# Performance work log

Measured on AMD Instinct MI355X. Metric: run time of the kernel, lower is better.

## Reference

```python
import jax, jax.numpy as jnp
import numpy as np

B, S, D = 2, 2048, 2048
H, KVH = 32, 8
HD = D // H          # 64
N_REP = H // KVH     # 4
NEG = -1e9


def setup_inputs() -> dict:
    key = jax.random.key(0)
    ks = jax.random.split(key, 5)
    x = jax.random.normal(ks[0], (B, S, D), dtype=jnp.float32)
    std = 0.02
    wq = jax.random.normal(ks[1], (H * HD, D), dtype=jnp.float32) * std
    wk = jax.random.normal(ks[2], (KVH * HD, D), dtype=jnp.float32) * std
    wv = jax.random.normal(ks[3], (KVH * HD, D), dtype=jnp.float32) * std
    wo = jax.random.normal(ks[4], (D, H * HD), dtype=jnp.float32) * std
    # RoPE tables: (S, HD//2)
    inv_freq = 1.0 / (10000.0 ** (np.arange(0, HD, 2, dtype=np.float32) / HD))
    t = np.arange(S, dtype=np.float32)
    freqs = np.outer(t, inv_freq)
    freqs_cos = jnp.asarray(np.cos(freqs))
    freqs_sin = jnp.asarray(np.sin(freqs))
    # additive causal mask [1,1,S,S]
    causal = np.tril(np.ones((S, S), dtype=bool))
    mask = jnp.asarray(np.where(causal, 0.0, NEG).astype(np.float32))[None, None]
    return {"x": x, "wq": wq, "wk": wk, "wv": wv, "wo": wo,
            "freqs_cos": freqs_cos, "freqs_sin": freqs_sin, "mask": mask}


def _apply_rope(t, cos, sin):
    # t: [B,S,nh,HD]; cos/sin: [S, HD//2]
    tr = t.reshape(t.shape[:-1] + (HD // 2, 2))
    r, i = tr[..., 0], tr[..., 1]
    c = cos[None, :, None, :]
    s = sin[None, :, None, :]
    out_r = r * c - i * s
    out_i = r * s + i * c
    return jnp.stack([out_r, out_i], axis=-1).reshape(t.shape)


def reference(x, wq, wk, wv, wo, freqs_cos, freqs_sin, mask):
    b, s, _ = x.shape
    q = (x @ wq.T).reshape(b, s, H, HD)
    k = (x @ wk.T).reshape(b, s, KVH, HD)
    v = (x @ wv.T).reshape(b, s, KVH, HD)
    q = _apply_rope(q, freqs_cos, freqs_sin)
    k = _apply_rope(k, freqs_cos, freqs_sin)
    # repeat_kv (GQA expansion) then move heads forward: [B,H,S,HD]
    k = jnp.repeat(k, N_REP, axis=2)
    v = jnp.repeat(v, N_REP, axis=2)
    q = q.transpose(0, 2, 1, 3)
    k = k.transpose(0, 2, 1, 3)
    v = v.transpose(0, 2, 1, 3)
    scale = 1.0 / jnp.sqrt(jnp.float32(HD))
    scores = jnp.einsum("bhqd,bhkd->bhqk", q, k) * scale + mask[:, :, :s, :s]
    attn = jax.nn.softmax(scores, axis=-1)
    out = jnp.einsum("bhqk,bhkd->bhqd", attn, v)
    out = out.transpose(0, 2, 1, 3).reshape(b, s, H * HD)
    return out @ wo.T
```

## Files before the change

### kernel.cpp

```cpp
#include <hip/hip_runtime.h>
#include <hip/hip_bf16.h>
#include <stdint.h>


#define NEG_BIG (-1e9f)
#define SCALE_LOG2 0.18033688011112042f
#define DEFER_THR 10.0f

typedef __bf16 bf16x8 __attribute__((ext_vector_type(8)));
typedef float f32x4 __attribute__((ext_vector_type(4)));
typedef float f32x16 __attribute__((ext_vector_type(16)));
typedef uint16_t u16x8 __attribute__((ext_vector_type(8)));
typedef uint32_t u32x4 __attribute__((ext_vector_type(4)));

__device__ inline uint16_t f2bf(float x) {
    __hip_bfloat16 h = __float2bfloat16(x);
    return __builtin_bit_cast(uint16_t, h);
}
__device__ inline float bf2f(uint16_t u) {
    uint32_t t = (uint32_t)u << 16;
    return __builtin_bit_cast(float, t);
}

__device__ inline void async_cp16(const void* g, void* l) {
    __builtin_amdgcn_global_load_lds(
        (const __attribute__((address_space(1))) uint32_t*)g,
        (__attribute__((address_space(3))) uint32_t*)l,
        16 , 0 , 0 );
}

__global__ void cvt4(const float* __restrict__ in, uint16_t* __restrict__ out, int n4) {
    int i = blockIdx.x * blockDim.x + threadIdx.x;
    if (i >= n4) return;
    const float4 v = ((const float4*)in)[i];
    ushort4 o;
    o.x = f2bf(v.x); o.y = f2bf(v.y); o.z = f2bf(v.z); o.w = f2bf(v.w);
    ((ushort4*)out)[i] = o;
}

__global__ void build_wqkv(const float* __restrict__ wq, const float* __restrict__ wk,
                           const float* __restrict__ wv, uint16_t* __restrict__ out) {
    int i = blockIdx.x * blockDim.x + threadIdx.x;
    if (i >= (3072 * 2048) / 4) return;
    int e = i * 4;
    int row = e >> 11;
    int col = e & 2047;
    const float* src = (row < 2048) ? (wq + (long)row * 2048 + col)
                     : (row < 2560) ? (wk + (long)(row - 2048) * 2048 + col)
                                    : (wv + (long)(row - 2560) * 2048 + col);
    const float4 v = *(const float4*)src;
    ushort4 o;
    o.x = f2bf(v.x); o.y = f2bf(v.y); o.z = f2bf(v.z); o.w = f2bf(v.w);
    ((ushort4*)(out + e))[0] = o;
}

template <int BN, int OUT_BF16>
__global__ __launch_bounds__(512) void gemm256(const uint16_t* __restrict__ A,
                                               const uint16_t* __restrict__ Bw,
                                               void* __restrict__ Cout,
                                               int M, int N, int K) {
    constexpr int WN = BN / 4;
    constexpr int NF = WN / 16;
    constexpr int BROUNDS = BN / 64;

    __shared__ __align__(16) uint16_t As[2][256 * 64];
    __shared__ __align__(16) uint16_t Bs[2][BN * 64];

    const int tid = threadIdx.x;
    const int l = tid & 63;
    const int w = tid >> 6;
    const int wmi = w >> 2;
    const int wni = w & 3;
    const int c = l & 15, g = l >> 4;
    const long row0 = (long)blockIdx.x * 256;
    const long col0 = (long)blockIdx.y * BN;

    f32x4 acc[8][NF] = {};

    auto STAGE = [&](int buf, int t) {
        const long k0 = (long)t * 64;
#pragma unroll
        for (int rr = 0; rr < 4; ++rr) {
            const int e = rr * 512 + tid;
            const int r = e >> 3;
            const int gs = (e & 7) ^ (r & 7);
            async_cp16(A + (row0 + r) * (long)K + k0 + gs * 8, &As[buf][e * 8]);
        }
#pragma unroll
        for (int rr = 0; rr < BROUNDS; ++rr) {
            const int e = rr * 512 + tid;
            const int r = e >> 3;
            const int gs = (e & 7) ^ (r & 7);
            async_cp16(Bw + (col0 + r) * (long)K + k0 + gs * 8, &Bs[buf][e * 8]);
        }
    };

    STAGE(0, 0);
    __syncthreads();

    const int nt = K / 64;
    for (int t = 0; t < nt; ++t) {
        const int cur = t & 1;
        if (t + 1 < nt) STAGE(cur ^ 1, t + 1);

#pragma unroll
        for (int kk = 0; kk < 2; ++kk) {
            bf16x8 bF[NF];
#pragma unroll
            for (int n = 0; n < NF; ++n) {
                const int rb = wni * WN + n * 16 + c;
                const int sp = ((kk * 4 + g) ^ (c & 7));
                bF[n] = *(const bf16x8*)&Bs[cur][rb * 64 + sp * 8];
            }
#pragma unroll
            for (int mh = 0; mh < 2; ++mh) {
                bf16x8 aF[4];
#pragma unroll
                for (int mm = 0; mm < 4; ++mm) {
                    const int ra = wmi * 128 + (mh * 4 + mm) * 16 + c;
                    const int sp = ((kk * 4 + g) ^ (c & 7));
                    aF[mm] = *(const bf16x8*)&As[cur][ra * 64 + sp * 8];
                }
                __builtin_amdgcn_s_setprio(1);
#pragma unroll
                for (int mm = 0; mm < 4; ++mm)
#pragma unroll
                    for (int n = 0; n < NF; ++n)
                        acc[mh * 4 + mm][n] = __builtin_amdgcn_mfma_f32_16x16x32_bf16(
                            aF[mm], bF[n], acc[mh * 4 + mm][n], 0, 0, 0);
                __builtin_amdgcn_s_setprio(0);
            }
        }
        if (t + 1 < nt) __syncthreads();
    }

#pragma unroll
    for (int m = 0; m < 8; ++m) {
        const long rg = row0 + wmi * 128 + m * 16 + g * 4;
#pragma unroll
        for (int n = 0; n < NF; ++n) {
            const long cg = col0 + wni * WN + n * 16 + c;
#pragma unroll
            for (int r = 0; r < 4; ++r) {
                float v = acc[m][n][r];
                if (OUT_BF16)
                    ((uint16_t*)Cout)[(rg + r) * (long)N + cg] = f2bf(v);
                else
                    ((float*)Cout)[(rg + r) * (long)N + cg] = v;
            }
        }
    }
}

__global__ void rope_q(uint16_t* __restrict__ qkv,
                       const float* __restrict__ cosT,
                       const float* __restrict__ sinT) {
    int idx = blockIdx.x * blockDim.x + threadIdx.x;
    if (idx >= 4096 * 1024) return;
    int m = idx >> 10;
    int j = idx & 1023;
    int s = m & 2047;
    int d2 = j & 31;
    float cc = cosT[s * 32 + d2];
    float ss = sinT[s * 32 + d2];
    uint32_t* p = (uint32_t*)(qkv + (long)m * 3072 + 2 * j);
    uint32_t v = *p;
    float re = bf2f((uint16_t)(v & 0xffffu));
    float im = bf2f((uint16_t)(v >> 16));
    float orr = re * cc - im * ss;
    float oi = re * ss + im * cc;
    *p = (uint32_t)f2bf(orr) | ((uint32_t)f2bf(oi) << 16);
}

__global__ void kpack_rope(const uint16_t* __restrict__ qkv,
                           const float* __restrict__ cosT,
                           const float* __restrict__ sinT,
                           uint16_t* __restrict__ Kpk) {
    const int wid = (blockIdx.x * blockDim.x + threadIdx.x) >> 6;
    const int l = threadIdx.x & 63;
    const int lq = l & 31, hi = l >> 5;
    const int s = wid & 3;
    const int tile = (wid >> 2) & 63;
    const int bk = wid >> 8;
    const int b = bk >> 3, kvh = bk & 7;
    const int key = 32 * tile + lq;
    const uint16_t* src = qkv + (long)(b * 2048 + key) * 3072
                        + 2048 + kvh * 64 + 16 * s + 8 * hi;
    u16x8 v = *(const u16x8*)src;
    const int d2b = 8 * s + 4 * hi;
    u16x8 o;
#pragma unroll
    for (int p = 0; p < 4; ++p) {
        const float cc = cosT[key * 32 + d2b + p];
        const float ss = sinT[key * 32 + d2b + p];
        const float re = bf2f(v[2 * p]);
        const float im = bf2f(v[2 * p + 1]);
        o[2 * p]     = f2bf(re * cc - im * ss);
        o[2 * p + 1] = f2bf(re * ss + im * cc);
    }
    *(u16x8*)(Kpk + (((long)(bk * 64 + tile) * 4 + s) * 64 + l) * 8) = o;
}

__global__ void vpack_direct(const uint16_t* __restrict__ qkv, uint16_t* __restrict__ Vpk) {
    const int wid = (blockIdx.x * blockDim.x + threadIdx.x) >> 6;
    const int l = threadIdx.x & 63;
    const int lq = l & 31, hi = l >> 5;
    const int s2 = wid & 1;
    const int nd = (wid >> 1) & 1;
    const int tile = (wid >> 2) & 63;
    const int bk = wid >> 8;
    const int b = bk >> 3, kvh = bk & 7;
    const int key0 = 32 * tile + 16 * s2 + 8 * hi;
    const uint16_t* src = qkv + (long)(b * 2048 + key0) * 3072
                        + 2560 + kvh * 64 + nd * 32 + lq;
    u16x8 v;
#pragma unroll
    for (int jj = 0; jj < 8; ++jj) v[jj] = src[(long)jj * 3072];
    *(u16x8*)(Vpk + ((((long)(bk * 64 + tile) * 2 + nd) * 2 + s2) * 64 + l) * 8) = v;
}

__device__ inline void pack_pf(const float pr[16], int hi, bf16x8 pf[2]) {
    uint32_t wds[8], xw[8];
#pragma unroll
    for (int m = 0; m < 8; ++m)
        wds[m] = (uint32_t)f2bf(pr[2 * m]) | ((uint32_t)f2bf(pr[2 * m + 1]) << 16);
#pragma unroll
    for (int m = 0; m < 8; ++m)
        xw[m] = (uint32_t)__shfl_xor((int)wds[m], 32);
#pragma unroll
    for (int s = 0; s < 2; ++s) {
        u32x4 pk;
        pk[0] = hi ? xw[4 * s + 2] : wds[4 * s + 0];
        pk[1] = hi ? xw[4 * s + 3] : wds[4 * s + 1];
        pk[2] = hi ? wds[4 * s + 2] : xw[4 * s + 0];
        pk[3] = hi ? wds[4 * s + 3] : xw[4 * s + 1];
        pf[s] = __builtin_bit_cast(bf16x8, pk);
    }
}

__global__ __launch_bounds__(128) void attn_fwd(const uint16_t* __restrict__ qkv,
                                                const uint16_t* __restrict__ Kpk,
                                                const uint16_t* __restrict__ Vpk,
                                                uint16_t* __restrict__ outb) {
    const int bid = blockIdx.x;
    const int bhp = bid & 31;
    const int j = 63 - (bid >> 5);
    const int t0 = threadIdx.x;
    const int l = t0 & 63, ww = t0 >> 6;
    const int gh = 2 * bhp + ww;
    const int b = gh >> 5, h = gh & 31;
    const int kvh = h >> 2;
    const int bk = b * 8 + kvh;
    const int lq = l & 31, hi = l >> 5;
    const int q = 32 * j + lq;

    const uint16_t* qrow = qkv + (long)(b * 2048 + q) * 3072 + h * 64 + 8 * hi;
    bf16x8 qf[4];
#pragma unroll
    for (int s = 0; s < 4; ++s) qf[s] = *(const bf16x8*)(qrow + 16 * s);

    float m_run = -1e30f, l_run = 0.f;
    f32x16 accO[2] = {};

    const uint16_t* kbase = Kpk + (long)bk * 64 * 2048 + (long)l * 8;
    const uint16_t* vbase = Vpk + (long)bk * 64 * 2048 + (long)l * 8;
    const int nT = (j + 2) >> 1;

    for (int t = 0; t < nT; ++t) {
        bf16x8 kf[2][4];
#pragma unroll
        for (int u = 0; u < 2; ++u)
#pragma unroll
            for (int s = 0; s < 4; ++s)
                kf[u][s] = *(const bf16x8*)(kbase + (long)(2 * t + u) * 2048 + s * 512);

        f32x16 st0 = {}, st1 = {};
        __builtin_amdgcn_s_setprio(1);
#pragma unroll
        for (int s = 0; s < 4; ++s)
            st0 = __builtin_amdgcn_mfma_f32_32x32x16_bf16(kf[0][s], qf[s], st0, 0, 0, 0);
#pragma unroll
        for (int s = 0; s < 4; ++s)
            st1 = __builtin_amdgcn_mfma_f32_32x32x16_bf16(kf[1][s], qf[s], st1, 0, 0, 0);
        __builtin_amdgcn_s_setprio(0);

        bf16x8 vf[2][2][2];
#pragma unroll
        for (int u = 0; u < 2; ++u)
#pragma unroll
            for (int nd = 0; nd < 2; ++nd)
#pragma unroll
                for (int s2 = 0; s2 < 2; ++s2)
                    vf[u][nd][s2] = *(const bf16x8*)(vbase + (long)(2 * t + u) * 2048 + nd * 1024 + s2 * 512);

        float sc0[16], sc1[16];
        if (t == nT - 1) {
            const int tq0 = lq + ((j - 2 * t) << 5) - 4 * hi;
            const int tq1 = tq0 - 32;
#pragma unroll
            for (int r = 0; r < 16; ++r) {
                const int kc = (r & 3) + 8 * (r >> 2);
                sc0[r] = st0[r] * SCALE_LOG2 + (kc > tq0 ? NEG_BIG : 0.f);
                sc1[r] = st1[r] * SCALE_LOG2 + (kc > tq1 ? NEG_BIG : 0.f);
            }
        } else {
#pragma unroll
            for (int r = 0; r < 16; ++r) {
                sc0[r] = st0[r] * SCALE_LOG2;
                sc1[r] = st1[r] * SCALE_LOG2;
            }
        }

        float vm = sc0[0];
#pragma unroll
        for (int r = 1; r < 16; ++r) vm = fmaxf(vm, sc0[r]);
#pragma unroll
        for (int r = 0; r < 16; ++r) vm = fmaxf(vm, sc1[r]);
        vm = fmaxf(vm, __shfl_xor(vm, 32));
        if (!__all(vm - m_run <= DEFER_THR)) {
            const float mnew = fmaxf(m_run, vm);
            const float alpha = __builtin_amdgcn_exp2f(m_run - mnew);
            m_run = mnew;
            l_run *= alpha;
#pragma unroll
            for (int nd = 0; nd < 2; ++nd)
#pragma unroll
                for (int r = 0; r < 16; ++r) accO[nd][r] *= alpha;
        }

        float pr0[16], pr1[16];
        float sum = 0.f;
#pragma unroll
        for (int r = 0; r < 16; ++r) {
            pr0[r] = __builtin_amdgcn_exp2f(sc0[r] - m_run);
            sum += pr0[r];
        }
#pragma unroll
        for (int r = 0; r < 16; ++r) {
            pr1[r] = __builtin_amdgcn_exp2f(sc1[r] - m_run);
            sum += pr1[r];
        }
        sum += __shfl_xor(sum, 32);
        l_run += sum;

        bf16x8 pf0[2], pf1[2];
        pack_pf(pr0, hi, pf0);
        pack_pf(pr1, hi, pf1);

        __builtin_amdgcn_s_setprio(1);
#pragma unroll
        for (int nd = 0; nd < 2; ++nd) {
            accO[nd] = __builtin_amdgcn_mfma_f32_32x32x16_bf16(vf[0][nd][0], pf0[0], accO[nd], 0, 0, 0);
            accO[nd] = __builtin_amdgcn_mfma_f32_32x32x16_bf16(vf[0][nd][1], pf0[1], accO[nd], 0, 0, 0);
            accO[nd] = __builtin_amdgcn_mfma_f32_32x32x16_bf16(vf[1][nd][0], pf1[0], accO[nd], 0, 0, 0);
            accO[nd] = __builtin_amdgcn_mfma_f32_32x32x16_bf16(vf[1][nd][1], pf1[1], accO[nd], 0, 0, 0);
        }
        __builtin_amdgcn_s_setprio(0);
    }

    const float invl = 1.0f / l_run;
    uint16_t* orow = outb + (long)(b * 2048 + q) * 2048 + h * 64 + 4 * hi;
#pragma unroll
    for (int nd = 0; nd < 2; ++nd)
#pragma unroll
        for (int m = 0; m < 4; ++m) {
            ushort4 o;
            o.x = f2bf(accO[nd][4 * m + 0] * invl);
            o.y = f2bf(accO[nd][4 * m + 1] * invl);
            o.z = f2bf(accO[nd][4 * m + 2] * invl);
            o.w = f2bf(accO[nd][4 * m + 3] * invl);
            *(ushort4*)(orow + nd * 32 + 8 * m) = o;
        }
}

extern "C" void kernel_launch(void* const* d_in, const int* in_sizes, int n_in,
                              void* d_out, int out_size, void* d_ws, size_t ws_size,
                              hipStream_t stream) {
    const float* x    = (const float*)d_in[0];
    const float* wq   = (const float*)d_in[1];
    const float* wk   = (const float*)d_in[2];
    const float* wv   = (const float*)d_in[3];
    const float* wo   = (const float*)d_in[4];
    const float* fcos = (const float*)d_in[5];
    const float* fsin = (const float*)d_in[6];
    float* out = (float*)d_out;

    uint8_t* ws = (uint8_t*)d_ws;
    const size_t MiB = 1048576;
    uint16_t* x_bf   = (uint16_t*)(ws);
    uint16_t* w_bf   = (uint16_t*)(ws + 16 * MiB);
    uint16_t* qkv_bf = (uint16_t*)(ws + 28 * MiB);
    uint16_t* att_bf = x_bf;
    uint16_t* Kpk    = (uint16_t*)(ws + 16 * MiB);
    uint16_t* Vpk    = (uint16_t*)(ws + 20 * MiB);
    uint16_t* wo_bf  = (uint16_t*)(ws + 16 * MiB);

    cvt4<<<(2097152 + 255) / 256, 256, 0, stream>>>(x, x_bf, 2097152);
    build_wqkv<<<(1572864 + 255) / 256, 256, 0, stream>>>(wq, wk, wv, w_bf);

    gemm256<256, 1><<<dim3(16, 12), 512, 0, stream>>>(x_bf, w_bf, qkv_bf, 4096, 3072, 2048);

    rope_q<<<16384, 256, 0, stream>>>(qkv_bf, fcos, fsin);
    kpack_rope<<<1024, 256, 0, stream>>>(qkv_bf, fcos, fsin, Kpk);
    vpack_direct<<<1024, 256, 0, stream>>>(qkv_bf, Vpk);

    attn_fwd<<<2048, 128, 0, stream>>>(qkv_bf, Kpk, Vpk, att_bf);

    cvt4<<<(1048576 + 255) / 256, 256, 0, stream>>>(wo, wo_bf, 1048576);
    gemm256<128, 0><<<dim3(16, 16), 512, 0, stream>>>(att_bf, wo_bf, out, 4096, 2048, 2048);
}
```

Baseline: 221.9 us.

## Fold softmax scale into Q RoPE, merge K/V pack kernels, retile QKV GEMM

Pre-scales Q by scale*log2(e) inside the RoPE kernel, so the attention loop no longer multiplies every score and only applies the causal mask on the diagonal tile. The max and sum reductions become tree-shaped to shorten dependency chains. The separate K-pack and V-pack launches are merged into one kernel to save a launch. The QKV GEMM moves to a 192-wide N tile with a 16x16 grid for better CU coverage. Rounding Q to bf16 after scaling changes numerics slightly.

```diff
diff --git a/kernel.cpp b/kernel.cpp
--- a/kernel.cpp
+++ b/kernel.cpp
@@ -167,56 +167,56 @@
     uint32_t v = *p;
     float re = bf2f((uint16_t)(v & 0xffffu));
     float im = bf2f((uint16_t)(v >> 16));
-    float orr = re * cc - im * ss;
-    float oi = re * ss + im * cc;
+    float orr = (re * cc - im * ss) * SCALE_LOG2;
+    float oi  = (re * ss + im * cc) * SCALE_LOG2;
     *p = (uint32_t)f2bf(orr) | ((uint32_t)f2bf(oi) << 16);
 }
 
-__global__ void kpack_rope(const uint16_t* __restrict__ qkv,
-                           const float* __restrict__ cosT,
-                           const float* __restrict__ sinT,
-                           uint16_t* __restrict__ Kpk) {
-    const int wid = (blockIdx.x * blockDim.x + threadIdx.x) >> 6;
+__global__ void pack_kv(const uint16_t* __restrict__ qkv,
+                        const float* __restrict__ cosT,
+                        const float* __restrict__ sinT,
+                        uint16_t* __restrict__ Kpk,
+                        uint16_t* __restrict__ Vpk) {
+    const int gw = (blockIdx.x * blockDim.x + threadIdx.x) >> 6;
     const int l = threadIdx.x & 63;
     const int lq = l & 31, hi = l >> 5;
-    const int s = wid & 3;
-    const int tile = (wid >> 2) & 63;
-    const int bk = wid >> 8;
-    const int b = bk >> 3, kvh = bk & 7;
-    const int key = 32 * tile + lq;
-    const uint16_t* src = qkv + (long)(b * 2048 + key) * 3072
-                        + 2048 + kvh * 64 + 16 * s + 8 * hi;
-    u16x8 v = *(const u16x8*)src;
-    const int d2b = 8 * s + 4 * hi;
-    u16x8 o;
-#pragma unroll
-    for (int p = 0; p < 4; ++p) {
-        const float cc = cosT[key * 32 + d2b + p];
-        const float ss = sinT[key * 32 + d2b + p];
-        const float re = bf2f(v[2 * p]);
-        const float im = bf2f(v[2 * p + 1]);
-        o[2 * p]     = f2bf(re * cc - im * ss);
-        o[2 * p + 1] = f2bf(re * ss + im * cc);
+    if (gw < 4096) {
+        const int wid = gw;
+        const int s = wid & 3;
+        const int tile = (wid >> 2) & 63;
+        const int bk = wid >> 8;
+        const int b = bk >> 3, kvh = bk & 7;
+        const int key = 32 * tile + lq;
+        const uint16_t* src = qkv + (long)(b * 2048 + key) * 3072
+                            + 2048 + kvh * 64 + 16 * s + 8 * hi;
+        u16x8 v = *(const u16x8*)src;
+        const int d2b = 8 * s + 4 * hi;
+        u16x8 o;
+#pragma unroll
+        for (int p = 0; p < 4; ++p) {
+            const float cc = cosT[key * 32 + d2b + p];
+            const float ss = sinT[key * 32 + d2b + p];
+            const float re = bf2f(v[2 * p]);
+            const float im = bf2f(v[2 * p + 1]);
+            o[2 * p]     = f2bf(re * cc - im * ss);
+            o[2 * p + 1] = f2bf(re * ss + im * cc);
+        }
+        *(u16x8*)(Kpk + (((long)(bk * 64 + tile) * 4 + s) * 64 + l) * 8) = o;
+    } else {
+        const int wid = gw - 4096;
+        const int s2 = wid & 1;
+        const int nd = (wid >> 1) & 1;
+        const int tile = (wid >> 2) & 63;
+        const int bk = wid >> 8;
+        const int b = bk >> 3, kvh = bk & 7;
+        const int key0 = 32 * tile + 16 * s2 + 8 * hi;
+        const uint16_t* src = qkv + (long)(b * 2048 + key0) * 3072
+                            + 2560 + kvh * 64 + nd * 32 + lq;
+        u16x8 v;
+#pragma unroll
+        for (int jj = 0; jj < 8; ++jj) v[jj] = src[(long)jj * 3072];
+        *(u16x8*)(Vpk + ((((long)(bk * 64 + tile) * 2 + nd) * 2 + s2) * 64 + l) * 8) = v;
     }
-    *(u16x8*)(Kpk + (((long)(bk * 64 + tile) * 4 + s) * 64 + l) * 8) = o;
-}
-
-__global__ void vpack_direct(const uint16_t* __restrict__ qkv, uint16_t* __restrict__ Vpk) {
-    const int wid = (blockIdx.x * blockDim.x + threadIdx.x) >> 6;
-    const int l = threadIdx.x & 63;
-    const int lq = l & 31, hi = l >> 5;
-    const int s2 = wid & 1;
-    const int nd = (wid >> 1) & 1;
-    const int tile = (wid >> 2) & 63;
-    const int bk = wid >> 8;
-    const int b = bk >> 3, kvh = bk & 7;
-    const int key0 = 32 * tile + 16 * s2 + 8 * hi;
-    const uint16_t* src = qkv + (long)(b * 2048 + key0) * 3072
-                        + 2560 + kvh * 64 + nd * 32 + lq;
-    u16x8 v;
-#pragma unroll
-    for (int jj = 0; jj < 8; ++jj) v[jj] = src[(long)jj * 3072];
-    *(u16x8*)(Vpk + ((((long)(bk * 64 + tile) * 2 + nd) * 2 + s2) * 64 + l) * 8) = v;
 }
 
 __device__ inline void pack_pf(const float pr[16], int hi, bf16x8 pf[2]) {
@@ -293,30 +293,27 @@
                 for (int s2 = 0; s2 < 2; ++s2)
                     vf[u][nd][s2] = *(const bf16x8*)(vbase + (long)(2 * t + u) * 2048 + nd * 1024 + s2 * 512);
 
-        float sc0[16], sc1[16];
         if (t == nT - 1) {
             const int tq0 = lq + ((j - 2 * t) << 5) - 4 * hi;
             const int tq1 = tq0 - 32;
 #pragma unroll
             for (int r = 0; r < 16; ++r) {
                 const int kc = (r & 3) + 8 * (r >> 2);
-                sc0[r] = st0[r] * SCALE_LOG2 + (kc > tq0 ? NEG_BIG : 0.f);
-                sc1[r] = st1[r] * SCALE_LOG2 + (kc > tq1 ? NEG_BIG : 0.f);
+                if (kc > tq0) st0[r] = NEG_BIG;
+                if (kc > tq1) st1[r] = NEG_BIG;
             }
-        } else {
-#pragma unroll
-            for (int r = 0; r < 16; ++r) {
-                sc0[r] = st0[r] * SCALE_LOG2;
-                sc1[r] = st1[r] * SCALE_LOG2;
-            }
-        }
-
-        float vm = sc0[0];
-#pragma unroll
-        for (int r = 1; r < 16; ++r) vm = fmaxf(vm, sc0[r]);
-#pragma unroll
-        for (int r = 0; r < 16; ++r) vm = fmaxf(vm, sc1[r]);
-        vm = fmaxf(vm, __shfl_xor(vm, 32));
+        }
+
+        float mx[16];
+#pragma unroll
+        for (int r = 0; r < 16; ++r) mx[r] = fmaxf(st0[r], st1[r]);
+#pragma unroll
+        for (int off = 8; off; off >>= 1)
+#pragma unroll
+            for (int r = 0; r < 8; ++r)
+                if (r < off) mx[r] = fmaxf(mx[r], mx[r + off]);
+        const float vm = fmaxf(mx[0], __shfl_xor(mx[0], 32));
+
         if (!__all(vm - m_run <= DEFER_THR)) {
             const float mnew = fmaxf(m_run, vm);
             const float alpha = __builtin_amdgcn_exp2f(m_run - mnew);
@@ -328,20 +325,20 @@
                 for (int r = 0; r < 16; ++r) accO[nd][r] *= alpha;
         }
 
-        float pr0[16], pr1[16];
-        float sum = 0.f;
-#pragma unroll
-        for (int r = 0; r < 16; ++r) {
-            pr0[r] = __builtin_amdgcn_exp2f(sc0[r] - m_run);
-            sum += pr0[r];
-        }
-#pragma unroll
-        for (int r = 0; r < 16; ++r) {
-            pr1[r] = __builtin_amdgcn_exp2f(sc1[r] - m_run);
-            sum += pr1[r];
-        }
-        sum += __shfl_xor(sum, 32);
-        l_run += sum;
+        float pr0[16], pr1[16], sm[8];
+#pragma unroll
+        for (int r = 0; r < 16; ++r) pr0[r] = __builtin_amdgcn_exp2f(st0[r] - m_run);
+#pragma unroll
+        for (int r = 0; r < 16; ++r) pr1[r] = __builtin_amdgcn_exp2f(st1[r] - m_run);
+#pragma unroll
+        for (int m = 0; m < 8; ++m)
+            sm[m] = (pr0[2 * m] + pr0[2 * m + 1]) + (pr1[2 * m] + pr1[2 * m + 1]);
+#pragma unroll
+        for (int off = 4; off; off >>= 1)
+#pragma unroll
+            for (int r = 0; r < 4; ++r)
+                if (r < off) sm[r] += sm[r + off];
+        l_run += sm[0] + __shfl_xor(sm[0], 32);
 
         bf16x8 pf0[2], pf1[2];
         pack_pf(pr0, hi, pf0);
@@ -398,11 +395,10 @@
     cvt4<<<(2097152 + 255) / 256, 256, 0, stream>>>(x, x_bf, 2097152);
     build_wqkv<<<(1572864 + 255) / 256, 256, 0, stream>>>(wq, wk, wv, w_bf);
 
-    gemm256<256, 1><<<dim3(16, 12), 512, 0, stream>>>(x_bf, w_bf, qkv_bf, 4096, 3072, 2048);
+    gemm256<192, 1><<<dim3(16, 16), 512, 0, stream>>>(x_bf, w_bf, qkv_bf, 4096, 3072, 2048);
 
     rope_q<<<16384, 256, 0, stream>>>(qkv_bf, fcos, fsin);
-    kpack_rope<<<1024, 256, 0, stream>>>(qkv_bf, fcos, fsin, Kpk);
-    vpack_direct<<<1024, 256, 0, stream>>>(qkv_bf, Vpk);
+    pack_kv<<<2048, 256, 0, stream>>>(qkv_bf, fcos, fsin, Kpk, Vpk);
 
     attn_fwd<<<2048, 128, 0, stream>>>(qkv_bf, Kpk, Vpk, att_bf);
 
```

Result: faster. 212.4 us (-4.3%).
